# Performance work log

Hardware: AMD Instinct MI355X
Metric: run time of the kernel (lower is better)

Reference implementation:

```python
import jax, jax.numpy as jnp
import numpy as np

N = 100000   # nodes
E = 800000   # edges
D = 128      # uniform hidden width
L = 3        # number of SAGE layers (len(hidden_channels)-1)
EPS = 1e-5   # BatchNorm eps


def setup_inputs() -> dict:
    key = jax.random.key(0)
    ks = jax.random.split(key, 7)
    s = 1.0 / np.sqrt(D)
    x = jax.random.normal(ks[0], (N, D), jnp.float32)
    edge_index = jax.random.randint(ks[1], (2, E), 0, N)
    Wl = jax.random.normal(ks[2], (L, D, D), jnp.float32) * s  # neighbor-branch weight (out,in)
    Wr = jax.random.normal(ks[3], (L, D, D), jnp.float32) * s  # root-branch weight (out,in)
    b = jax.random.normal(ks[4], (L, D), jnp.float32) * 0.01   # bias (lin_l only, PyG default)
    gamma = 1.0 + 0.1 * jax.random.normal(ks[5], (L, D), jnp.float32)
    beta = 0.1 * jax.random.normal(ks[6], (L, D), jnp.float32)
    return {"x": x, "edge_index": edge_index, "Wl": Wl, "Wr": Wr, "b": b,
            "gamma": gamma, "beta": beta}


def _sage(x, src, dst, Wl, Wr, b):
    # PyG SAGEConv: out = lin_l(mean_{j->i} x_j) + lin_r(x_i)
    agg = jax.ops.segment_sum(x[src], dst, num_segments=N)          # [N, D]
    cnt = jax.ops.segment_sum(jnp.ones((src.shape[0], 1), x.dtype), dst,
                              num_segments=N)                        # [N, 1]
    agg = agg / jnp.maximum(cnt, 1.0)  # mean; isolated nodes stay 0
    return agg @ Wl.T + x @ Wr.T + b


def _bn(x, g, be):
    # BatchNorm1d over the node axis, batch statistics, biased variance
    m = jnp.mean(x, axis=0)
    v = jnp.var(x, axis=0)
    return g * (x - m) * jax.lax.rsqrt(v + EPS) + be


def reference(x, edge_index, Wl, Wr, b, gamma, beta):
    src, dst = edge_index[0], edge_index[1]
    # hidden layers: SAGEConv -> ELU -> (dropout, eval no-op) -> BatchNorm
    for i in range(L - 1):
        h = jax.nn.elu(_sage(x, src, dst, Wl[i], Wr[i], b[i]))
        x = _bn(h, gamma[i], beta[i])
    # final layer: SAGEConv -> BatchNorm (no ELU/dropout)
    x = _bn(_sage(x, src, dst, Wl[L - 1], Wr[L - 1], b[L - 1]), gamma[L - 1], beta[L - 1])
    return x
```

## Files before the change

### kernel.cpp

```cpp
#include <hip/hip_runtime.h>
#include <hip/hip_bf16.h>

#define N_NODES 100000
#define N_EDGES 800000
#define DD 128
#define TILE 32
#define NBLK 3125
#define NSCAN1 391
#define EPSV 1e-5f
#define ECAP 768

typedef short bf16x8 __attribute__((ext_vector_type(8)));
typedef float f32x4 __attribute__((ext_vector_type(4)));

__device__ __forceinline__ short f2bf(float f) {
    unsigned u = __float_as_uint(f);
    unsigned r = (u + 0x7fffu + ((u >> 16) & 1u)) >> 16;
    return (short)r;
}
__device__ __forceinline__ float bf2f(short s) {
    return __uint_as_float(((unsigned)(unsigned short)s) << 16);
}

__global__ void k_setup(const float* __restrict__ x, short* __restrict__ xbf,
                        unsigned char* __restrict__ xq, float* __restrict__ xsc,
                        const int* __restrict__ dst, int* __restrict__ cnt) {
    int i = blockIdx.x * 256 + threadIdx.x;
    if (i < N_NODES * DD / 8) {
        f32x4 v0 = *(const f32x4*)(x + (size_t)i * 8);
        f32x4 v1 = *(const f32x4*)(x + (size_t)i * 8 + 4);
        float f[8] = {v0.x, v0.y, v0.z, v0.w, v1.x, v1.y, v1.z, v1.w};
        bf16x8 t;
#pragma unroll
        for (int j = 0; j < 8; ++j) t[j] = f2bf(f[j]);
        *(bf16x8*)&xbf[(size_t)i * 8] = t;

        float mx = 0.f;
#pragma unroll
        for (int j = 0; j < 8; ++j) mx = fmaxf(mx, fabsf(f[j]));
        mx = fmaxf(mx, __shfl_xor(mx, 1, 64));
        mx = fmaxf(mx, __shfl_xor(mx, 2, 64));
        mx = fmaxf(mx, __shfl_xor(mx, 4, 64));
        mx = fmaxf(mx, __shfl_xor(mx, 8, 64));
        float qi = mx > 0.f ? 127.f / mx : 0.f;
        unsigned w0 = 0, w1 = 0;
#pragma unroll
        for (int j = 0; j < 8; ++j) {
            int u = (int)rintf(f[j] * qi) + 128;
            u = min(max(u, 0), 255);
            if (j < 4) w0 |= (unsigned)u << (8 * j);
            else       w1 |= (unsigned)u << (8 * (j - 4));
        }
        uint2 pk; pk.x = w0; pk.y = w1;
        *(uint2*)&xq[(size_t)i * 8] = pk;
        if ((i & 15) == 0) xsc[i >> 4] = mx / 127.f;
    }
    if (i < N_EDGES) atomicAdd(&cnt[dst[i]], 1);
}

__global__ void k_scan1(const int* __restrict__ cnt, int* __restrict__ off,
                        int* __restrict__ bsums) {
    __shared__ int s[256];
    int i = blockIdx.x * 256 + threadIdx.x;
    int t = threadIdx.x;
    s[t] = (i < N_NODES) ? cnt[i] : 0;
    __syncthreads();
    for (int d = 1; d < 256; d <<= 1) {
        int x = 0;
        if (t >= d) x = s[t - d];
        __syncthreads();
        s[t] += x;
        __syncthreads();
    }
    if (i < N_NODES) off[i + 1] = s[t];
    if (t == 255) bsums[blockIdx.x] = s[255];
}

__global__ void k_scan2(int* __restrict__ bsums) {
    __shared__ int s[512];
    int t = threadIdx.x;
    s[t] = (t < NSCAN1) ? bsums[t] : 0;
    __syncthreads();
    for (int d = 1; d < 512; d <<= 1) {
        int x = 0;
        if (t >= d) x = s[t - d];
        __syncthreads();
        s[t] += x;
        __syncthreads();
    }
    if (t < NSCAN1) bsums[t] = s[t];
}

__global__ void k_scan3(int* __restrict__ off, const int* __restrict__ bsums) {
    int i = blockIdx.x * 256 + threadIdx.x;
    int add = (blockIdx.x > 0) ? bsums[blockIdx.x - 1] : 0;
    if (i < N_NODES) off[i + 1] += add;
    if (i == 0) off[0] = 0;
}

__global__ void k_fill(const int* __restrict__ src, const int* __restrict__ dst,
                       const int* __restrict__ off, int* __restrict__ cur,
                       int* __restrict__ elist) {
    int e = blockIdx.x * 256 + threadIdx.x;
    if (e < N_EDGES) {
        int d = dst[e];
        int p = atomicSub(&cur[d], 1);
        elist[off[d] + p - 1] = src[e];
    }
}

__global__ void k_fold(const float* __restrict__ wl, const float* __restrict__ wr,
                       const float* __restrict__ b, const float* __restrict__ aff,
                       int use_aff,
                       short* __restrict__ wblo, short* __restrict__ wbro,
                       float* __restrict__ bias_base, float* __restrict__ bias_deg) {
    int o = blockIdx.x;
    int k = threadIdx.x;
    float a = use_aff ? aff[k] : 1.f;
    float c = use_aff ? aff[128 + k] : 0.f;
    float vl = wl[o * DD + k], vr = wr[o * DD + k];
    wblo[o * DD + k] = f2bf(vl * a);
    wbro[o * DD + k] = f2bf(vr * a);
    __shared__ float s1[128], s2[128];
    s1[k] = c * vr; s2[k] = c * vl;
    __syncthreads();
    for (int d = 64; d > 0; d >>= 1) {
        if (k < d) { s1[k] += s1[k + d]; s2[k] += s2[k + d]; }
        __syncthreads();
    }
    if (k == 0) {
        bias_base[o] = b[o] + s1[0];
        bias_deg[o] = s2[0];
    }
}

template <bool ELU_ON, bool WQ>
__global__ __launch_bounds__(256, 8) void k_sage(
    short* __restrict__ xb,
    const unsigned char* __restrict__ gq,
    const float* __restrict__ gsc,
    unsigned char* __restrict__ hq,
    float* __restrict__ hsc,
    const int* __restrict__ off, const int* __restrict__ elist,
    const short* __restrict__ wl, const short* __restrict__ wr,
    const float* __restrict__ bias_base, const float* __restrict__ bias_deg,
    float* __restrict__ partials)
{
    __shared__ short agg_t[TILE * 128];
    __shared__ float sstat[4 * 128];
    __shared__ int soff[TILE + 1];
    __shared__ int eidx[ECAP];
    const int tid = threadIdx.x;
    const int wu = __builtin_amdgcn_readfirstlane(tid >> 6);
    const int l = tid & 63;
    const int base = blockIdx.x * TILE;
    const int qw = l >> 4;
    const int ll = l & 15;

    if (tid < TILE + 1) soff[tid] = off[min(base + tid, N_NODES)];
    __syncthreads();
    const int ebase = soff[0];
    const int etot = soff[TILE] - ebase;
    const bool ovf = etot > ECAP;
    for (int k = tid; k < (ovf ? 0 : etot); k += 256) eidx[k] = elist[ebase + k];
    __syncthreads();
    const int* ep = ovf ? (elist + ebase) : (const int*)eidx;

#pragma unroll
    for (int q = 0; q < 2; ++q) {
        const int m = wu * 8 + q * 4 + qw;
        const int ea = soff[m] - ebase;
        const int eA = soff[m + 1] - ebase;
        const int deg = eA - ea;
        float acc[8];
        float ssum = 0.f;
#pragma unroll
        for (int j = 0; j < 8; ++j) acc[j] = 0.f;

        uint2 v0{}, v1{}, v2{}, v3{}, v4{}, v5{}, v6{}, v7{};
        float s0f = 0.f, s1f = 0.f, s2f = 0.f, s3f = 0.f;
        float s4f = 0.f, s5f = 0.f, s6f = 0.f, s7f = 0.f;
        int e = ea;
#define GLOAD(sn) (*(const uint2*)(gq + (size_t)(sn) * DD + 8 * ll))
#define ACC(v, s) { ssum += (s); \
        acc[0] += (s) * (float)((v).x & 0xffu); \
        acc[1] += (s) * (float)(((v).x >> 8) & 0xffu); \
        acc[2] += (s) * (float)(((v).x >> 16) & 0xffu); \
        acc[3] += (s) * (float)((v).x >> 24); \
        acc[4] += (s) * (float)((v).y & 0xffu); \
        acc[5] += (s) * (float)(((v).y >> 8) & 0xffu); \
        acc[6] += (s) * (float)(((v).y >> 16) & 0xffu); \
        acc[7] += (s) * (float)((v).y >> 24); }
#define PRIME(d) if (e + d < eA) { int sn = ep[e + d]; v##d = GLOAD(sn); s##d##f = gsc[sn]; }
        PRIME(0) PRIME(1) PRIME(2) PRIME(3) PRIME(4) PRIME(5) PRIME(6) PRIME(7)
#define STEP(d) if (e + d < eA) { ACC(v##d, s##d##f) \
        int en = e + 8 + d; \
        if (en < eA) { int sn = ep[en]; v##d = GLOAD(sn); s##d##f = gsc[sn]; } }
        while (__any((int)(e < eA))) {
            STEP(0) STEP(1) STEP(2) STEP(3) STEP(4) STEP(5) STEP(6) STEP(7)
            e += 8;
        }
#undef STEP
#undef PRIME
#undef ACC
#undef GLOAD

        float inv = deg > 0 ? 1.f / (float)deg : 0.f;
        bf16x8 t;
#pragma unroll
        for (int j = 0; j < 8; ++j) t[j] = f2bf((acc[j] - 128.f * ssum) * inv);
        *(bf16x8*)&agg_t[m * DD + ((8 * ll) ^ ((m & 7) << 3))] = t;
    }
    __syncthreads();

    const int p = wu >> 1;
    const int half = wu & 1;
    f32x4 acc[4];
#pragma unroll
    for (int nb = 0; nb < 4; ++nb) acc[nb] = f32x4{0.f, 0.f, 0.f, 0.f};
    const int mrow = p * 16 + (l & 15);
    const int kg = (l >> 4) * 8;
    const int nloc = l & 15;
    const int groot = min(base + mrow, N_NODES - 1);
#pragma unroll
    for (int ks = 0; ks < 4; ++ks) {
        int kk = ks * 32 + kg;
        int sw = kk ^ ((mrow & 7) << 3);
        bf16x8 aa = *(const bf16x8*)&agg_t[mrow * DD + sw];
        bf16x8 ax = *(const bf16x8*)(xb + (size_t)groot * DD + kk);
#pragma unroll
        for (int nb = 0; nb < 4; ++nb) {
            int n = half * 64 + nb * 16 + nloc;
            bf16x8 bl = *(const bf16x8*)&wl[n * DD + kk];
            bf16x8 br = *(const bf16x8*)&wr[n * DD + kk];
            acc[nb] = __builtin_amdgcn_mfma_f32_16x16x32_bf16(aa, bl, acc[nb], 0, 0, 0);
            acc[nb] = __builtin_amdgcn_mfma_f32_16x16x32_bf16(ax, br, acc[nb], 0, 0, 0);
        }
    }
    __syncthreads();

    int degf[4];
#pragma unroll
    for (int r = 0; r < 4; ++r) {
        int mr_ = p * 16 + (l >> 4) * 4 + r;
        degf[r] = soff[mr_ + 1] - soff[mr_];
    }

    float colS[4], colQ[4];
#pragma unroll
    for (int nb = 0; nb < 4; ++nb) {
        int n = half * 64 + nb * 16 + nloc;
        float bb = bias_base[n];
        float bd = bias_deg[n];
        float cs = 0.f, cq = 0.f;
#pragma unroll
        for (int r = 0; r < 4; ++r) {
            int m = p * 16 + (l >> 4) * 4 + r;
            int g = base + m;
            float hv = acc[nb][r] + bb + (degf[r] > 0 ? bd : 0.f);
            if (ELU_ON) hv = hv > 0.f ? hv : expm1f(hv);
            agg_t[m * DD + (n ^ ((m & 7) << 3))] = f2bf(hv);
            float hm = (g < N_NODES) ? hv : 0.f;
            cs += hm;
            cq += hm * hm;
        }
        colS[nb] = cs; colQ[nb] = cq;
    }
#pragma unroll
    for (int nb = 0; nb < 4; ++nb) {
        colS[nb] += __shfl_xor(colS[nb], 16, 64);
        colS[nb] += __shfl_xor(colS[nb], 32, 64);
        colQ[nb] += __shfl_xor(colQ[nb], 16, 64);
        colQ[nb] += __shfl_xor(colQ[nb], 32, 64);
    }
    if (l < 16) {
#pragma unroll
        for (int nb = 0; nb < 4; ++nb) {
            sstat[wu * 128 + nb * 16 + l]      = colS[nb];
            sstat[wu * 128 + 64 + nb * 16 + l] = colQ[nb];
        }
    }
    __syncthreads();

#pragma unroll
    for (int k = 0; k < 2; ++k) {
        int idx = (k * 256 + tid) * 8;
        int m = idx >> 7, c = idx & 127;
        int g = base + m;
        bf16x8 v = *(const bf16x8*)&agg_t[m * DD + (c ^ ((m & 7) << 3))];
        *(bf16x8*)&xb[(size_t)g * DD + c] = v;
        if (WQ) {
            float f[8];
#pragma unroll
            for (int j = 0; j < 8; ++j) f[j] = bf2f(v[j]);
            float mx = 0.f;
#pragma unroll
            for (int j = 0; j < 8; ++j) mx = fmaxf(mx, fabsf(f[j]));
            mx = fmaxf(mx, __shfl_xor(mx, 1, 64));
            mx = fmaxf(mx, __shfl_xor(mx, 2, 64));
            mx = fmaxf(mx, __shfl_xor(mx, 4, 64));
            mx = fmaxf(mx, __shfl_xor(mx, 8, 64));
            float qi = mx > 0.f ? 127.f / mx : 0.f;
            unsigned w0 = 0, w1 = 0;
#pragma unroll
            for (int j = 0; j < 8; ++j) {
                int u = (int)rintf(f[j] * qi) + 128;
                u = min(max(u, 0), 255);
                if (j < 4) w0 |= (unsigned)u << (8 * j);
                else       w1 |= (unsigned)u << (8 * (j - 4));
            }
            uint2 pk; pk.x = w0; pk.y = w1;
            *(uint2*)&hq[(size_t)g * DD + c] = pk;
            if ((tid & 15) == 0) hsc[g] = mx / 127.f;
        }
    }
    {
        int f = tid & 127;
        int part = tid >> 7;
        int hsel = f >> 6;
        int cw = part * 64 + (f & 63);
        float v = 0.f;
#pragma unroll
        for (int pr = 0; pr < 2; ++pr) v += sstat[(2 * pr + hsel) * 128 + cw];
        partials[blockIdx.x * 256 + tid] = v;
    }
}

__global__ void k_reduce(const float* __restrict__ partials,
                         const float* __restrict__ gamma, const float* __restrict__ beta,
                         float* __restrict__ aff) {
    int f = blockIdx.x;
    int t = threadIdx.x;
    float s = 0.f, q = 0.f;
    for (int i = t; i < NBLK; i += 256) {
        s += partials[i * 256 + f];
        q += partials[i * 256 + 128 + f];
    }
    __shared__ float rs[256], rq[256];
    rs[t] = s; rq[t] = q;
    __syncthreads();
    for (int d = 128; d > 0; d >>= 1) {
        if (t < d) { rs[t] += rs[t + d]; rq[t] += rq[t + d]; }
        __syncthreads();
    }
    if (t == 0) {
        float mean = rs[0] / (float)N_NODES;
        float var = rq[0] / (float)N_NODES - mean * mean;
        float a = gamma[f] * rsqrtf(var + EPSV);
        aff[f] = a;
        aff[128 + f] = beta[f] - mean * a;
    }
}

__global__ void k_apply(const short* __restrict__ hin, const float* __restrict__ aff,
                        float* __restrict__ out) {
    int i = blockIdx.x * 256 + threadIdx.x;
    if (i < N_NODES * DD / 8) {
        bf16x8 v = *(const bf16x8*)(hin + (size_t)i * 8);
        int f = (i * 8) & 127;
        f32x4 a0 = *(const f32x4*)(aff + f);
        f32x4 a1 = *(const f32x4*)(aff + f + 4);
        f32x4 c0 = *(const f32x4*)(aff + 128 + f);
        f32x4 c1 = *(const f32x4*)(aff + 128 + f + 4);
        f32x4 o0, o1;
        o0.x = bf2f(v[0]) * a0.x + c0.x; o0.y = bf2f(v[1]) * a0.y + c0.y;
        o0.z = bf2f(v[2]) * a0.z + c0.z; o0.w = bf2f(v[3]) * a0.w + c0.w;
        o1.x = bf2f(v[4]) * a1.x + c1.x; o1.y = bf2f(v[5]) * a1.y + c1.y;
        o1.z = bf2f(v[6]) * a1.z + c1.z; o1.w = bf2f(v[7]) * a1.w + c1.w;
        *(f32x4*)(out + (size_t)i * 8) = o0;
        *(f32x4*)(out + (size_t)i * 8 + 4) = o1;
    }
}

extern "C" void kernel_launch(void* const* d_in, const int* in_sizes, int n_in,
                              void* d_out, int out_size, void* d_ws, size_t ws_size,
                              hipStream_t stream) {
    const float* x     = (const float*)d_in[0];
    const int*   ei    = (const int*)d_in[1];
    const float* Wl    = (const float*)d_in[2];
    const float* Wr    = (const float*)d_in[3];
    const float* b     = (const float*)d_in[4];
    const float* gamma = (const float*)d_in[5];
    const float* beta  = (const float*)d_in[6];
    float* out = (float*)d_out;

    char* ws = (char*)d_ws;
    int*   off      = (int*)(ws + 0);
    int*   cnt      = (int*)(ws + 400128);
    int*   elist    = (int*)(ws + 800256);
    int*   bsums    = (int*)(ws + 4000256);
    float* partials = (float*)(ws + 4002304);
    float* affine   = (float*)(ws + 7202304);
    short* wbl      = (short*)(ws + 7203328);
    short* wbr      = (short*)(ws + 7236096);
    float* biasb    = (float*)(ws + 7268864);
    float* biasd    = (float*)(ws + 7269376);
    short* xb       = (short*)(ws + 7269888);
    unsigned char* qA = (unsigned char*)(ws + 32869888);
    unsigned char* qB = (unsigned char*)(ws + 45669888);
    float* scA = (float*)d_out;
    float* scB = (float*)cnt;

    const int* src = ei;
    const int* dst = ei + N_EDGES;

    hipMemsetAsync(cnt, 0, N_NODES * sizeof(int), stream);
    k_setup<<<(N_NODES * DD / 8 + 255) / 256, 256, 0, stream>>>(x, xb, qA, scA, dst, cnt);
    k_scan1<<<NSCAN1, 256, 0, stream>>>(cnt, off, bsums);
    k_scan2<<<1, 512, 0, stream>>>(bsums);
    k_scan3<<<NSCAN1, 256, 0, stream>>>(off, bsums);
    k_fill<<<(N_EDGES + 255) / 256, 256, 0, stream>>>(src, dst, off, cnt, elist);

    k_fold<<<128, 128, 0, stream>>>(Wl, Wr, b, affine, 0, wbl, wbr, biasb, biasd);
    k_sage<true, true><<<NBLK, 256, 0, stream>>>(xb, qA, scA, qB, scB, off, elist,
                                                 wbl, wbr, biasb, biasd, partials);
    k_reduce<<<128, 256, 0, stream>>>(partials, gamma, beta, affine);

    k_fold<<<128, 128, 0, stream>>>(Wl + DD * DD, Wr + DD * DD, b + DD, affine, 1,
                                    wbl, wbr, biasb, biasd);
    k_sage<true, true><<<NBLK, 256, 0, stream>>>(xb, qB, scB, qA, scA, off, elist,
                                                 wbl, wbr, biasb, biasd, partials);
    k_reduce<<<128, 256, 0, stream>>>(partials, gamma + DD, beta + DD, affine);

    k_fold<<<128, 128, 0, stream>>>(Wl + 2 * DD * DD, Wr + 2 * DD * DD, b + 2 * DD,
                                    affine, 1, wbl, wbr, biasb, biasd);
    k_sage<false, false><<<NBLK, 256, 0, stream>>>(xb, qA, scA, qB, scB, off, elist,
                                                   wbl, wbr, biasb, biasd, partials);
    k_reduce<<<128, 256, 0, stream>>>(partials, gamma + 2 * DD, beta + 2 * DD, affine);

    k_apply<<<(N_NODES * DD / 8 + 255) / 256, 256, 0, stream>>>(xb, affine, out);
}
```

Before: 484.0 us.

## Gather neighbor rows into LDS via global_load_lds with double-buffered chunks

The per-row register-prefetch gather is replaced by a per-wave scheme. Each wave processes its 8 destination rows as one contiguous edge stream and issues async global_load_lds copies of 16 quantized neighbor rows per chunk, double-buffered in LDS, with the per-edge scales also loaded into LDS. Each lane then accumulates 2 columns across the edges and flushes a row when an edge boundary is crossed. The intent is to raise memory-level parallelism and balance work across uneven degrees, at the cost of extra LDS use (which may lower occupancy), full vmcnt waits between chunks, and a slow scalar fallback for waves with more than 128 edges.

```diff
diff --git a/kernel.cpp b/kernel.cpp
--- a/kernel.cpp
+++ b/kernel.cpp
@@ -9,8 +9,10 @@
 #define NSCAN1 391
 #define EPSV 1e-5f
 #define ECAP 768
+#define WCAP 128
 
 typedef short bf16x8 __attribute__((ext_vector_type(8)));
+typedef short bf16x2 __attribute__((ext_vector_type(2)));
 typedef float f32x4 __attribute__((ext_vector_type(4)));
 
 __device__ __forceinline__ short f2bf(float f) {
@@ -20,6 +22,10 @@
 }
 __device__ __forceinline__ float bf2f(short s) {
     return __uint_as_float(((unsigned)(unsigned short)s) << 16);
+}
+
+__device__ __forceinline__ void gll4(const void* g, void* l) {
+    __builtin_amdgcn_global_load_lds((const unsigned int*)g, (unsigned int*)l, 4, 0, 0);
 }
 
 __global__ void k_setup(const float* __restrict__ x, short* __restrict__ xbf,
@@ -150,12 +156,12 @@
     __shared__ float sstat[4 * 128];
     __shared__ int soff[TILE + 1];
     __shared__ int eidx[ECAP];
+    __shared__ float scb[4][WCAP];
+    __shared__ unsigned char rowb[4][2][16 * 128];
     const int tid = threadIdx.x;
     const int wu = __builtin_amdgcn_readfirstlane(tid >> 6);
     const int l = tid & 63;
     const int base = blockIdx.x * TILE;
-    const int qw = l >> 4;
-    const int ll = l & 15;
 
     if (tid < TILE + 1) soff[tid] = off[min(base + tid, N_NODES)];
     __syncthreads();
@@ -166,50 +172,93 @@
     __syncthreads();
     const int* ep = ovf ? (elist + ebase) : (const int*)eidx;
 
-#pragma unroll
-    for (int q = 0; q < 2; ++q) {
-        const int m = wu * 8 + q * 4 + qw;
-        const int ea = soff[m] - ebase;
-        const int eA = soff[m + 1] - ebase;
-        const int deg = eA - ea;
-        float acc[8];
-        float ssum = 0.f;
-#pragma unroll
-        for (int j = 0; j < 8; ++j) acc[j] = 0.f;
-
-        uint2 v0{}, v1{}, v2{}, v3{}, v4{}, v5{}, v6{}, v7{};
-        float s0f = 0.f, s1f = 0.f, s2f = 0.f, s3f = 0.f;
-        float s4f = 0.f, s5f = 0.f, s6f = 0.f, s7f = 0.f;
-        int e = ea;
-#define GLOAD(sn) (*(const uint2*)(gq + (size_t)(sn) * DD + 8 * ll))
-#define ACC(v, s) { ssum += (s); \
-        acc[0] += (s) * (float)((v).x & 0xffu); \
-        acc[1] += (s) * (float)(((v).x >> 8) & 0xffu); \
-        acc[2] += (s) * (float)(((v).x >> 16) & 0xffu); \
-        acc[3] += (s) * (float)((v).x >> 24); \
-        acc[4] += (s) * (float)((v).y & 0xffu); \
-        acc[5] += (s) * (float)(((v).y >> 8) & 0xffu); \
-        acc[6] += (s) * (float)(((v).y >> 16) & 0xffu); \
-        acc[7] += (s) * (float)((v).y >> 24); }
-#define PRIME(d) if (e + d < eA) { int sn = ep[e + d]; v##d = GLOAD(sn); s##d##f = gsc[sn]; }
-        PRIME(0) PRIME(1) PRIME(2) PRIME(3) PRIME(4) PRIME(5) PRIME(6) PRIME(7)
-#define STEP(d) if (e + d < eA) { ACC(v##d, s##d##f) \
-        int en = e + 8 + d; \
-        if (en < eA) { int sn = ep[en]; v##d = GLOAD(sn); s##d##f = gsc[sn]; } }
-        while (__any((int)(e < eA))) {
-            STEP(0) STEP(1) STEP(2) STEP(3) STEP(4) STEP(5) STEP(6) STEP(7)
-            e += 8;
-        }
-#undef STEP
-#undef PRIME
-#undef ACC
-#undef GLOAD
-
-        float inv = deg > 0 ? 1.f / (float)deg : 0.f;
-        bf16x8 t;
-#pragma unroll
-        for (int j = 0; j < 8; ++j) t[j] = f2bf((acc[j] - 128.f * ssum) * inv);
-        *(bf16x8*)&agg_t[m * DD + ((8 * ll) ^ ((m & 7) << 3))] = t;
+    {
+        const int wrow = wu * 8;
+        const int sofl = soff[wrow + min(l, 8)];
+        const int ew0 = __builtin_amdgcn_readlane(sofl, 0);
+        const int ew8 = __builtin_amdgcn_readlane(sofl, 8);
+        const int eaw = ew0 - ebase;
+        const int Ew = ew8 - ew0;
+
+        float a0 = 0.f, a1 = 0.f, ss = 0.f;
+        int r = 0;
+
+#define FLUSHROW() { \
+        int db0_ = __builtin_amdgcn_readlane(sofl, r); \
+        int db1_ = __builtin_amdgcn_readlane(sofl, r + 1); \
+        int dg_ = db1_ - db0_; \
+        float inv_ = dg_ > 0 ? 1.f / (float)dg_ : 0.f; \
+        bf16x2 t_; \
+        t_[0] = f2bf((a0 - 128.f * ss) * inv_); \
+        t_[1] = f2bf((a1 - 128.f * ss) * inv_); \
+        int m_ = wrow + r; \
+        int ci_ = m_ * DD + ((((l >> 2) ^ (m_ & 7)) << 3) | ((2 * l) & 7)); \
+        *(bf16x2*)&agg_t[ci_] = t_; \
+        a0 = 0.f; a1 = 0.f; ss = 0.f; }
+
+        if (Ew > 0) {
+            const int idxA = ep[min(eaw + l, eaw + Ew - 1)];
+            const int idxB = ep[min(eaw + 64 + l, eaw + Ew - 1)];
+            gll4(gsc + idxA, &scb[wu][0]);
+            if (Ew > 64) gll4(gsc + idxB, &scb[wu][64]);
+            const int C = min((Ew + 15) >> 4, 8);
+
+#define ISSUE_CHUNK(c_) { \
+            unsigned char* rb_ = &rowb[wu][(c_) & 1][0]; \
+            _Pragma("unroll") \
+            for (int i_ = 0; i_ < 8; ++i_) { \
+                int lsa_ = (c_) * 16 + 2 * i_; \
+                int sA_ = lsa_ < 64 ? __builtin_amdgcn_readlane(idxA, lsa_) \
+                                    : __builtin_amdgcn_readlane(idxB, lsa_ - 64); \
+                int sB_ = lsa_ + 1 < 64 ? __builtin_amdgcn_readlane(idxA, lsa_ + 1) \
+                                        : __builtin_amdgcn_readlane(idxB, lsa_ - 63); \
+                int sn_ = (l < 32) ? sA_ : sB_; \
+                gll4(gq + (size_t)sn_ * DD + (l & 31) * 4, rb_ + i_ * 256); \
+            } }
+
+            ISSUE_CHUNK(0)
+            if (C > 1) ISSUE_CHUNK(1)
+            int bnd = __builtin_amdgcn_readlane(sofl, 1) - ew0;
+            for (int c = 0; c < C; ++c) {
+                asm volatile("s_waitcnt vmcnt(0)" ::: "memory");
+                __builtin_amdgcn_sched_barrier(0);
+                const unsigned char* rb_ = &rowb[wu][c & 1][0];
+                const int jend = min(16, Ew - c * 16);
+                for (int j = 0; j < jend; ++j) {
+                    const int e = c * 16 + j;
+                    while (e >= bnd) {
+                        FLUSHROW();
+                        ++r;
+                        bnd = __builtin_amdgcn_readlane(sofl, r + 1) - ew0;
+                    }
+                    unsigned u = *(const unsigned short*)(rb_ + j * 128 + 2 * l);
+                    float s = scb[wu][e];
+                    a0 += s * (float)(u & 0xffu);
+                    a1 += s * (float)(u >> 8);
+                    ss += s;
+                }
+                if (c + 2 < C) {
+                    asm volatile("s_waitcnt lgkmcnt(0)" ::: "memory");
+                    ISSUE_CHUNK(c + 2)
+                }
+            }
+            for (int e = WCAP; e < Ew; ++e) {
+                while (e >= bnd) {
+                    FLUSHROW();
+                    ++r;
+                    bnd = __builtin_amdgcn_readlane(sofl, r + 1) - ew0;
+                }
+                int sn = ep[eaw + e];
+                float s = gsc[sn];
+                unsigned u = *(const unsigned short*)(gq + (size_t)sn * DD + 2 * l);
+                a0 += s * (float)(u & 0xffu);
+                a1 += s * (float)(u >> 8);
+                ss += s;
+            }
+#undef ISSUE_CHUNK
+        }
+        while (r < 8) { FLUSHROW(); ++r; }
+#undef FLUSHROW
     }
     __syncthreads();
 
@@ -241,9 +290,9 @@
 
     int degf[4];
 #pragma unroll
-    for (int r = 0; r < 4; ++r) {
-        int mr_ = p * 16 + (l >> 4) * 4 + r;
-        degf[r] = soff[mr_ + 1] - soff[mr_];
+    for (int rr = 0; rr < 4; ++rr) {
+        int mr_ = p * 16 + (l >> 4) * 4 + rr;
+        degf[rr] = soff[mr_ + 1] - soff[mr_];
     }
 
     float colS[4], colQ[4];
@@ -254,10 +303,10 @@
         float bd = bias_deg[n];
         float cs = 0.f, cq = 0.f;
 #pragma unroll
-        for (int r = 0; r < 4; ++r) {
-            int m = p * 16 + (l >> 4) * 4 + r;
+        for (int rr = 0; rr < 4; ++rr) {
+            int m = p * 16 + (l >> 4) * 4 + rr;
             int g = base + m;
-            float hv = acc[nb][r] + bb + (degf[r] > 0 ? bd : 0.f);
+            float hv = acc[nb][rr] + bb + (degf[rr] > 0 ? bd : 0.f);
             if (ELU_ON) hv = hv > 0.f ? hv : expm1f(hv);
             agg_t[m * DD + (n ^ ((m & 7) << 3))] = f2bf(hv);
             float hm = (g < N_NODES) ? hv : 0.f;
```

Measured after the change: 428.7 us. 1.13x faster.

## Gather neighbors with one wavefront per edge stream across its 8 rows

Applied to the files above, without the earlier changes.

The aggregation gather is restructured so each wavefront walks the combined edge list of its 8 destination rows, with all 64 lanes reading 2 bytes each of one neighbor's 128-byte quantized row. Before, 16 lanes each loaded 8 bytes per node, with four nodes per wave and two passes. The goal is to remove the lane divergence that came from uneven degrees within a wave and to make each neighbor load a single fully coalesced 128-byte access. In exchange, each edge now costs more serialized per-lane work, the prefetch depth drops to 4, and row boundaries add flush branches.

```diff
diff --git a/kernel.cpp b/kernel.cpp
--- a/kernel.cpp
+++ b/kernel.cpp
@@ -11,6 +11,7 @@
 #define ECAP 768
 
 typedef short bf16x8 __attribute__((ext_vector_type(8)));
+typedef short bf16x2 __attribute__((ext_vector_type(2)));
 typedef float f32x4 __attribute__((ext_vector_type(4)));
 
 __device__ __forceinline__ short f2bf(float f) {
@@ -154,8 +155,6 @@
     const int wu = __builtin_amdgcn_readfirstlane(tid >> 6);
     const int l = tid & 63;
     const int base = blockIdx.x * TILE;
-    const int qw = l >> 4;
-    const int ll = l & 15;
 
     if (tid < TILE + 1) soff[tid] = off[min(base + tid, N_NODES)];
     __syncthreads();
@@ -166,50 +165,48 @@
     __syncthreads();
     const int* ep = ovf ? (elist + ebase) : (const int*)eidx;
 
-#pragma unroll
-    for (int q = 0; q < 2; ++q) {
-        const int m = wu * 8 + q * 4 + qw;
-        const int ea = soff[m] - ebase;
-        const int eA = soff[m + 1] - ebase;
-        const int deg = eA - ea;
-        float acc[8];
-        float ssum = 0.f;
-#pragma unroll
-        for (int j = 0; j < 8; ++j) acc[j] = 0.f;
-
-        uint2 v0{}, v1{}, v2{}, v3{}, v4{}, v5{}, v6{}, v7{};
+    {
+        const int wrow = wu * 8;
+        const int e0 = soff[wrow] - ebase;
+        const int e1 = soff[wrow + 8] - ebase;
+        float a0 = 0.f, a1 = 0.f, ss = 0.f;
+        int r = 0;
+        int bnd = soff[wrow + 1] - ebase;
+
+        unsigned v0 = 0, v1 = 0, v2 = 0, v3 = 0;
         float s0f = 0.f, s1f = 0.f, s2f = 0.f, s3f = 0.f;
-        float s4f = 0.f, s5f = 0.f, s6f = 0.f, s7f = 0.f;
-        int e = ea;
-#define GLOAD(sn) (*(const uint2*)(gq + (size_t)(sn) * DD + 8 * ll))
-#define ACC(v, s) { ssum += (s); \
-        acc[0] += (s) * (float)((v).x & 0xffu); \
-        acc[1] += (s) * (float)(((v).x >> 8) & 0xffu); \
-        acc[2] += (s) * (float)(((v).x >> 16) & 0xffu); \
-        acc[3] += (s) * (float)((v).x >> 24); \
-        acc[4] += (s) * (float)((v).y & 0xffu); \
-        acc[5] += (s) * (float)(((v).y >> 8) & 0xffu); \
-        acc[6] += (s) * (float)(((v).y >> 16) & 0xffu); \
-        acc[7] += (s) * (float)((v).y >> 24); }
-#define PRIME(d) if (e + d < eA) { int sn = ep[e + d]; v##d = GLOAD(sn); s##d##f = gsc[sn]; }
-        PRIME(0) PRIME(1) PRIME(2) PRIME(3) PRIME(4) PRIME(5) PRIME(6) PRIME(7)
-#define STEP(d) if (e + d < eA) { ACC(v##d, s##d##f) \
-        int en = e + 8 + d; \
-        if (en < eA) { int sn = ep[en]; v##d = GLOAD(sn); s##d##f = gsc[sn]; } }
-        while (__any((int)(e < eA))) {
-            STEP(0) STEP(1) STEP(2) STEP(3) STEP(4) STEP(5) STEP(6) STEP(7)
-            e += 8;
-        }
-#undef STEP
-#undef PRIME
-#undef ACC
-#undef GLOAD
-
-        float inv = deg > 0 ? 1.f / (float)deg : 0.f;
-        bf16x8 t;
-#pragma unroll
-        for (int j = 0; j < 8; ++j) t[j] = f2bf((acc[j] - 128.f * ssum) * inv);
-        *(bf16x8*)&agg_t[m * DD + ((8 * ll) ^ ((m & 7) << 3))] = t;
+
+#define GLOADW(sn) ((unsigned)*(const unsigned short*)(gq + (size_t)(sn) * DD + 2 * l))
+#define PRIMEW(d) if (e0 + d < e1) { \
+        int sn = __builtin_amdgcn_readfirstlane(ep[e0 + d]); \
+        v##d = GLOADW(sn); s##d##f = gsc[sn]; }
+#define FLUSHW() { \
+        int dg_ = soff[wrow + r + 1] - soff[wrow + r]; \
+        float inv_ = dg_ > 0 ? 1.f / (float)dg_ : 0.f; \
+        bf16x2 t_; \
+        t_[0] = f2bf((a0 - 128.f * ss) * inv_); \
+        t_[1] = f2bf((a1 - 128.f * ss) * inv_); \
+        int m_ = wrow + r; \
+        *(bf16x2*)&agg_t[m_ * DD + ((((l >> 2) ^ (m_ & 7)) << 3) | ((2 * l) & 7))] = t_; \
+        a0 = 0.f; a1 = 0.f; ss = 0.f; }
+#define STEPW(d) if (e + d < e1) { \
+        while (e + d >= bnd) { FLUSHW(); ++r; bnd = soff[wrow + r + 1] - ebase; } \
+        a0 += s##d##f * (float)(v##d & 0xffu); \
+        a1 += s##d##f * (float)(v##d >> 8); \
+        ss += s##d##f; \
+        if (e + d + 4 < e1) { \
+            int sn = __builtin_amdgcn_readfirstlane(ep[e + d + 4]); \
+            v##d = GLOADW(sn); s##d##f = gsc[sn]; } }
+
+        PRIMEW(0) PRIMEW(1) PRIMEW(2) PRIMEW(3)
+        for (int e = e0; e < e1; e += 4) {
+            STEPW(0) STEPW(1) STEPW(2) STEPW(3)
+        }
+        while (r < 8) { FLUSHW(); ++r; }
+#undef STEPW
+#undef FLUSHW
+#undef PRIMEW
+#undef GLOADW
     }
     __syncthreads();
 
@@ -241,9 +238,9 @@
 
     int degf[4];
 #pragma unroll
-    for (int r = 0; r < 4; ++r) {
-        int mr_ = p * 16 + (l >> 4) * 4 + r;
-        degf[r] = soff[mr_ + 1] - soff[mr_];
+    for (int rr = 0; rr < 4; ++rr) {
+        int mr_ = p * 16 + (l >> 4) * 4 + rr;
+        degf[rr] = soff[mr_ + 1] - soff[mr_];
     }
 
     float colS[4], colQ[4];
@@ -254,10 +251,10 @@
         float bd = bias_deg[n];
         float cs = 0.f, cq = 0.f;
 #pragma unroll
-        for (int r = 0; r < 4; ++r) {
-            int m = p * 16 + (l >> 4) * 4 + r;
+        for (int rr = 0; rr < 4; ++rr) {
+            int m = p * 16 + (l >> 4) * 4 + rr;
             int g = base + m;
-            float hv = acc[nb][r] + bb + (degf[r] > 0 ? bd : 0.f);
+            float hv = acc[nb][rr] + bb + (degf[rr] > 0 ? bd : 0.f);
             if (ELU_ON) hv = hv > 0.f ? hv : expm1f(hv);
             agg_t[m * DD + (n ^ ((m & 7) << 3))] = f2bf(hv);
             float hm = (g < N_NODES) ? hv : 0.f;
```

Result: no change. 491.2 us (+1.5%).
